# Kernel optimization log

Hardware: AMD Instinct MI355X
Metric: run time of the kernel (lower is better)

Reference implementation:

```python
import jax, jax.numpy as jnp
import numpy as np


def setup_inputs() -> dict:
    key = jax.random.key(0)
    ks = jax.random.split(key, 9)
    B, C, H, W = 16, 512, 64, 64
    C8 = C // 8
    s_in = 1.0 / np.sqrt(C)
    s_out = 1.0 / np.sqrt(C8)
    return {
        "x": jax.random.normal(ks[0], (B, C, H, W), dtype=jnp.float32),
        "Wq": jax.random.normal(ks[1], (C8, C), dtype=jnp.float32) * s_in,
        "bq": jax.random.normal(ks[2], (C8,), dtype=jnp.float32) * s_in,
        "Wk": jax.random.normal(ks[3], (C8, C), dtype=jnp.float32) * s_in,
        "bk": jax.random.normal(ks[4], (C8,), dtype=jnp.float32) * s_in,
        "Wv": jax.random.normal(ks[5], (C8, C), dtype=jnp.float32) * s_in,
        "bv": jax.random.normal(ks[6], (C8,), dtype=jnp.float32) * s_in,
        "Wo": jax.random.normal(ks[7], (C, C8), dtype=jnp.float32) * s_out,
        "bo": jax.random.normal(ks[8], (C,), dtype=jnp.float32) * s_out,
    }


def reference(x, Wq, bq, Wk, bk, Wv, bv, Wo, bo):
    B, C, H, W = x.shape
    N = H * W
    xf = x.reshape(B, C, N)  # 1x1 conv == channel matmul over flattened spatial
    q = jnp.einsum("oc,bcn->bon", Wq, xf) + bq[None, :, None]  # [B, C8, N]
    k = jnp.einsum("oc,bcn->bon", Wk, xf) + bk[None, :, None]
    v = jnp.einsum("oc,bcn->bon", Wv, xf) + bv[None, :, None]
    energy = jnp.einsum("bcn,bdn->bcd", q, k)  # [B, C8, C8] channel attention
    attn = jax.nn.softmax(energy, axis=-1)
    out = jnp.einsum("bcd,bdn->bcn", attn, v)  # [B, C8, N]
    out = jnp.einsum("oc,bcn->bon", Wo, out) + bo[None, :, None]  # [B, C, N]
    return out.reshape(B, C, H, W)
```

## Files before the change

kernel.cpp:

```cpp
#include <hip/hip_runtime.h>
#include <hip/hip_bf16.h>
#include <cstdint>

#define B_SZ 16
#define C_IN 512
#define C8   64
#define NSP  4096
#define QR   192

typedef __attribute__((ext_vector_type(8))) short s8v;
typedef __attribute__((ext_vector_type(4))) float f4v;

__device__ __forceinline__ void split_bf16(float x, unsigned short& h, unsigned short& l) {
    unsigned int u = __float_as_uint(x);
    h = (unsigned short)(u >> 16);
    float r = x - __uint_as_float(u & 0xffff0000u);
    l = (unsigned short)(__float_as_uint(r) >> 16);
}

__global__ __launch_bounds__(256) void k_convW(
    const float* __restrict__ Wq, const float* __restrict__ Wk,
    const float* __restrict__ Wv,
    unsigned short* __restrict__ whi, unsigned short* __restrict__ wlo)
{
    const int o = blockIdx.x;
    const float* src = (o < 64)  ? (Wq + (size_t)o * C_IN)
                     : (o < 128) ? (Wk + (size_t)(o - 64) * C_IN)
                                 : (Wv + (size_t)(o - 128) * C_IN);
    for (int c = threadIdx.x; c < C_IN; c += 256) {
        unsigned short h, l;
        split_bf16(src[c], h, l);
        whi[(size_t)o * C_IN + c] = h;
        wlo[(size_t)o * C_IN + c] = l;
    }
}

__global__ __launch_bounds__(512, 4) void k_qkv_mfma(
    const float* __restrict__ x,
    const unsigned short* __restrict__ whi, const unsigned short* __restrict__ wlo,
    const float* __restrict__ bq, const float* __restrict__ bk,
    const float* __restrict__ bv,
    float* __restrict__ qkv)
{
    __shared__ unsigned short as_h[QR * 32], as_l[QR * 32];
    __shared__ unsigned short xs_h[128 * 32], xs_l[128 * 32];

    const int b  = blockIdx.y;
    const int n0 = blockIdx.x * 128;
    const int t  = threadIdx.x;
    const int w  = t >> 6;
    const int l  = t & 63;
    const int wm = w >> 1;
    const int wn = w & 1;
    const int lm = l & 15;
    const int slot = (((l >> 4) ^ (l & 3)) << 3);

    const int nB    = t & 127;
    const int kgB   = t >> 7;
    const int slotB = ((kgB ^ (nB & 3)) << 3);

    f4v acc[3][4];
#pragma unroll
    for (int i = 0; i < 3; ++i)
#pragma unroll
        for (int j = 0; j < 4; ++j) acc[i][j] = (f4v)0.f;

    const float* xcol = x + ((size_t)b * C_IN) * NSP + n0 + nB;
    float xr[8];
    auto loadB = [&](int K0) {
        const float* s_ = xcol + (size_t)(K0 + kgB * 8) * NSP;
#pragma unroll
        for (int j = 0; j < 8; ++j) xr[j] = s_[(size_t)j * NSP];
    };
    loadB(0);

    for (int it = 0; it < 16; ++it) {
        const int k0 = it * 32;
        __syncthreads();
        {
            unsigned short h[8], lo[8];
#pragma unroll
            for (int j = 0; j < 8; ++j) split_bf16(xr[j], h[j], lo[j]);
            s8v hv, lv;
#pragma unroll
            for (int j = 0; j < 8; ++j) { hv[j] = (short)h[j]; lv[j] = (short)lo[j]; }
            *(s8v*)&xs_h[nB * 32 + slotB] = hv;
            *(s8v*)&xs_l[nB * 32 + slotB] = lv;
        }
        for (int c = t; c < 768; c += 512) {
            const int m = c >> 2, kga = c & 3;
            const int dst = m * 32 + ((kga ^ (m & 3)) << 3);
            const size_t srcoff = (size_t)m * C_IN + k0 + kga * 8;
            *(s8v*)&as_h[dst] = *(const s8v*)&whi[srcoff];
            *(s8v*)&as_l[dst] = *(const s8v*)&wlo[srcoff];
        }
        if (it < 15) loadB(k0 + 32);
        __syncthreads();
        s8v ah[3], al[3], bh[4], bl[4];
#pragma unroll
        for (int fm = 0; fm < 3; ++fm) {
            const int m = wm * 48 + fm * 16 + lm;
            ah[fm] = *(const s8v*)&as_h[m * 32 + slot];
            al[fm] = *(const s8v*)&as_l[m * 32 + slot];
        }
#pragma unroll
        for (int fn = 0; fn < 4; ++fn) {
            const int n = wn * 64 + fn * 16 + lm;
            bh[fn] = *(const s8v*)&xs_h[n * 32 + slot];
            bl[fn] = *(const s8v*)&xs_l[n * 32 + slot];
        }
#pragma unroll
        for (int fm = 0; fm < 3; ++fm)
#pragma unroll
            for (int fn = 0; fn < 4; ++fn) {
                acc[fm][fn] = __builtin_amdgcn_mfma_f32_16x16x32_bf16(
                    ah[fm], bh[fn], acc[fm][fn], 0, 0, 0);
                acc[fm][fn] = __builtin_amdgcn_mfma_f32_16x16x32_bf16(
                    ah[fm], bl[fn], acc[fm][fn], 0, 0, 0);
                acc[fm][fn] = __builtin_amdgcn_mfma_f32_16x16x32_bf16(
                    al[fm], bh[fn], acc[fm][fn], 0, 0, 0);
            }
    }

#pragma unroll
    for (int fm = 0; fm < 3; ++fm) {
        const int row0 = wm * 48 + fm * 16;
        const float* barr = (row0 < 64) ? bq : (row0 < 128) ? bk : bv;
        const int rbase = (row0 & 63) + (l >> 4) * 4;
        const int rowg  = row0 + (l >> 4) * 4;
#pragma unroll
        for (int fn = 0; fn < 4; ++fn) {
            const int col = n0 + wn * 64 + fn * 16 + lm;
            float* dst = qkv + ((size_t)b * QR + rowg) * NSP + col;
#pragma unroll
            for (int r = 0; r < 4; ++r)
                dst[(size_t)r * NSP] = acc[fm][fn][r] + barr[rbase + r];
        }
    }
}

__global__ __launch_bounds__(256) void k_energy(
    const float* __restrict__ qkv, float* __restrict__ part)
{
    __shared__ float qs[64][133];
    __shared__ float ks[64][133];
    const int b = blockIdx.y, s = blockIdx.x;
    const int n0 = s * 128;
    const int t = threadIdx.x;
    const int cg = t & 15, dg = t >> 4;
    const float* qb = qkv + (size_t)b * QR * NSP + n0;
    const float* kb = qb + (size_t)C8 * NSP;
#pragma unroll
    for (int i = 0; i < 8; ++i) {
        int idx = t + 256 * i;
        int c = idx >> 5, j4 = idx & 31;
        float4 qv = *reinterpret_cast<const float4*>(qb + (size_t)c * NSP + j4 * 4);
        float4 kv = *reinterpret_cast<const float4*>(kb + (size_t)c * NSP + j4 * 4);
        qs[c][j4 * 4 + 0] = qv.x; qs[c][j4 * 4 + 1] = qv.y;
        qs[c][j4 * 4 + 2] = qv.z; qs[c][j4 * 4 + 3] = qv.w;
        ks[c][j4 * 4 + 0] = kv.x; ks[c][j4 * 4 + 1] = kv.y;
        ks[c][j4 * 4 + 2] = kv.z; ks[c][j4 * 4 + 3] = kv.w;
    }
    __syncthreads();
    float acc[4][4];
#pragma unroll
    for (int i = 0; i < 4; ++i)
#pragma unroll
        for (int j = 0; j < 4; ++j) acc[i][j] = 0.f;
#pragma unroll 4
    for (int nn = 0; nn < 128; ++nn) {
        float qv[4], kv[4];
#pragma unroll
        for (int i = 0; i < 4; ++i) qv[i] = qs[cg * 4 + i][nn];
#pragma unroll
        for (int j = 0; j < 4; ++j) kv[j] = ks[dg * 4 + j][nn];
#pragma unroll
        for (int i = 0; i < 4; ++i)
#pragma unroll
            for (int j = 0; j < 4; ++j)
                acc[i][j] = fmaf(qv[i], kv[j], acc[i][j]);
    }
#pragma unroll
    for (int i = 0; i < 4; ++i) {
        float4 ov;
        ov.x = acc[i][0]; ov.y = acc[i][1]; ov.z = acc[i][2]; ov.w = acc[i][3];
        *reinterpret_cast<float4*>(
            part + (((size_t)b * 32 + s) * 64 + cg * 4 + i) * 64 + dg * 4) = ov;
    }
}

__global__ __launch_bounds__(256) void k_softmax(
    const float* __restrict__ part, float* __restrict__ attn)
{
    __shared__ float red[4][64];
    const int cRow = blockIdx.x, b = blockIdx.y;
    const int t = threadIdx.x, d = t & 63, sg = t >> 6;
    const float* p = part + (size_t)b * 32 * 4096 + cRow * 64 + d;
    float s = 0.f;
#pragma unroll
    for (int i = 0; i < 8; ++i) s += p[(size_t)(sg * 8 + i) * 4096];
    red[sg][d] = s;
    __syncthreads();
    if (t < 64) {
        float v = red[0][d] + red[1][d] + red[2][d] + red[3][d];
        float m = v;
#pragma unroll
        for (int off = 32; off; off >>= 1) m = fmaxf(m, __shfl_xor(m, off));
        float e = __expf(v - m);
        float sum = e;
#pragma unroll
        for (int off = 32; off; off >>= 1) sum += __shfl_xor(sum, off);
        attn[((size_t)b * 64 + cRow) * 64 + d] = e / sum;
    }
}

__global__ __launch_bounds__(256) void k_woattn(
    const float* __restrict__ Wo, const float* __restrict__ attn,
    float* __restrict__ Mmat)
{
    __shared__ float wosT[64][68];
    __shared__ float as[64][68];
    const int b  = blockIdx.y;
    const int o0 = blockIdx.x * 64;
    const int t  = threadIdx.x;
    const int td = t & 15, to = t >> 4;
#pragma unroll
    for (int i = 0; i < 4; ++i) {
        int idx = t + 256 * i;
        int r = idx >> 4, q4 = idx & 15;
        float4 w = *reinterpret_cast<const float4*>(
            Wo + (size_t)(o0 + r) * 64 + q4 * 4);
        wosT[q4 * 4 + 0][r] = w.x; wosT[q4 * 4 + 1][r] = w.y;
        wosT[q4 * 4 + 2][r] = w.z; wosT[q4 * 4 + 3][r] = w.w;
        float4 a = *reinterpret_cast<const float4*>(
            attn + ((size_t)b * 64 + r) * 64 + q4 * 4);
        *reinterpret_cast<float4*>(&as[r][q4 * 4]) = a;
    }
    __syncthreads();
    float acc[4][4];
#pragma unroll
    for (int i = 0; i < 4; ++i)
#pragma unroll
        for (int j = 0; j < 4; ++j) acc[i][j] = 0.f;
#pragma unroll 8
    for (int kk = 0; kk < 64; ++kk) {
        float4 wv = *reinterpret_cast<const float4*>(&wosT[kk][to * 4]);
        float4 av = *reinterpret_cast<const float4*>(&as[kk][td * 4]);
        const float wr[4] = {wv.x, wv.y, wv.z, wv.w};
        const float ar[4] = {av.x, av.y, av.z, av.w};
#pragma unroll
        for (int i = 0; i < 4; ++i)
#pragma unroll
            for (int j = 0; j < 4; ++j)
                acc[i][j] = fmaf(wr[i], ar[j], acc[i][j]);
    }
#pragma unroll
    for (int i = 0; i < 4; ++i) {
        float4 ov;
        ov.x = acc[i][0]; ov.y = acc[i][1]; ov.z = acc[i][2]; ov.w = acc[i][3];
        *reinterpret_cast<float4*>(
            Mmat + ((size_t)b * 512 + o0 + to * 4 + i) * 64 + td * 4) = ov;
    }
}

__global__ __launch_bounds__(256) void k_out(
    const float* __restrict__ qkv, const float* __restrict__ Mmat,
    const float* __restrict__ bo, float* __restrict__ out)
{
    __shared__ float vs[64][68];
    __shared__ float msT[64][68];
    const int b  = blockIdx.z;
    const int o0 = blockIdx.y * 64;
    const int n0 = blockIdx.x * 64;
    const int t  = threadIdx.x;
    const int tn = t & 15, to = t >> 4;
    const float* vb = qkv + ((size_t)b * QR + 128) * NSP + n0;
#pragma unroll
    for (int i = 0; i < 4; ++i) {
        int idx = t + 256 * i;
        int r = idx >> 4, q4 = idx & 15;
        float4 v = *reinterpret_cast<const float4*>(vb + (size_t)r * NSP + q4 * 4);
        *reinterpret_cast<float4*>(&vs[r][q4 * 4]) = v;
        float4 m = *reinterpret_cast<const float4*>(
            Mmat + ((size_t)b * 512 + o0 + r) * 64 + q4 * 4);
        msT[q4 * 4 + 0][r] = m.x; msT[q4 * 4 + 1][r] = m.y;
        msT[q4 * 4 + 2][r] = m.z; msT[q4 * 4 + 3][r] = m.w;
    }
    __syncthreads();
    float acc[4][4];
#pragma unroll
    for (int i = 0; i < 4; ++i)
#pragma unroll
        for (int j = 0; j < 4; ++j) acc[i][j] = 0.f;
#pragma unroll 8
    for (int kk = 0; kk < 64; ++kk) {
        float4 mv = *reinterpret_cast<const float4*>(&msT[kk][to * 4]);
        float4 vv = *reinterpret_cast<const float4*>(&vs[kk][tn * 4]);
        const float mr[4] = {mv.x, mv.y, mv.z, mv.w};
        const float vr[4] = {vv.x, vv.y, vv.z, vv.w};
#pragma unroll
        for (int i = 0; i < 4; ++i)
#pragma unroll
            for (int j = 0; j < 4; ++j)
                acc[i][j] = fmaf(mr[i], vr[j], acc[i][j]);
    }
#pragma unroll
    for (int i = 0; i < 4; ++i) {
        int o = o0 + to * 4 + i;
        float bias = bo[o];
        float4 ov;
        ov.x = acc[i][0] + bias; ov.y = acc[i][1] + bias;
        ov.z = acc[i][2] + bias; ov.w = acc[i][3] + bias;
        *reinterpret_cast<float4*>(
            out + ((size_t)b * 512 + o) * NSP + n0 + tn * 4) = ov;
    }
}

extern "C" void kernel_launch(void* const* d_in, const int* in_sizes, int n_in,
                              void* d_out, int out_size, void* d_ws, size_t ws_size,
                              hipStream_t stream)
{
    const float* x  = (const float*)d_in[0];
    const float* Wq = (const float*)d_in[1];
    const float* bq = (const float*)d_in[2];
    const float* Wk = (const float*)d_in[3];
    const float* bk = (const float*)d_in[4];
    const float* Wv = (const float*)d_in[5];
    const float* bv = (const float*)d_in[6];
    const float* Wo = (const float*)d_in[7];
    const float* bo = (const float*)d_in[8];
    float* out = (float*)d_out;

    float* ws   = (float*)d_ws;
    float* qkv  = ws;
    float* part = qkv  + (size_t)B_SZ * QR * NSP;
    float* attn = part + (size_t)B_SZ * 32 * 64 * 64;
    float* Mmat = attn + (size_t)B_SZ * 64 * 64;

    unsigned short* whi = (unsigned short*)part;
    unsigned short* wlo = whi + (size_t)QR * C_IN;

    k_convW   <<<dim3(QR),          256, 0, stream>>>(Wq, Wk, Wv, whi, wlo);
    k_qkv_mfma<<<dim3(32, B_SZ),    512, 0, stream>>>(x, whi, wlo, bq, bk, bv, qkv);
    k_energy  <<<dim3(32, B_SZ),    256, 0, stream>>>(qkv, part);
    k_softmax <<<dim3(64, B_SZ),    256, 0, stream>>>(part, attn);
    k_woattn  <<<dim3(8, B_SZ),     256, 0, stream>>>(Wo, attn, Mmat);
    k_out     <<<dim3(64, 8, B_SZ), 256, 0, stream>>>(qkv, Mmat, bo, out);
}
```

Before: 333.6 us.

## Port energy and output projection kernels to split-bf16 MFMA

Rewrites the energy (Q·K^T partials) and final output projection kernels to use bf16 MFMA instructions with a hi/lo split (three MFMAs per tile) in place of scalar FP32 FMAs. The output kernel now stages V transposed as bf16 hi/lo in an XOR-swizzled shared-memory layout and processes 128 spatial columns per block. The aim is to cut the FP32 ALU cost of these GEMMs while keeping near-FP32 accuracy. It adds split conversion overhead, and the output stores are now scalar strided writes instead of float4.

```diff
diff --git a/kernel.cpp b/kernel.cpp
--- a/kernel.cpp
+++ b/kernel.cpp
@@ -16,6 +16,15 @@
     h = (unsigned short)(u >> 16);
     float r = x - __uint_as_float(u & 0xffff0000u);
     l = (unsigned short)(__float_as_uint(r) >> 16);
+}
+
+__device__ __forceinline__ void split8(const float* v, s8v& h, s8v& l) {
+#pragma unroll
+    for (int j = 0; j < 8; ++j) {
+        unsigned short hh, ll;
+        split_bf16(v[j], hh, ll);
+        h[j] = (short)hh; l[j] = (short)ll;
+    }
 }
 
 __global__ __launch_bounds__(256) void k_convW(
@@ -139,54 +148,46 @@
     }
 }
 
-__global__ __launch_bounds__(256) void k_energy(
+__global__ __launch_bounds__(256) void k_energy_mfma(
     const float* __restrict__ qkv, float* __restrict__ part)
 {
-    __shared__ float qs[64][133];
-    __shared__ float ks[64][133];
     const int b = blockIdx.y, s = blockIdx.x;
-    const int n0 = s * 128;
-    const int t = threadIdx.x;
-    const int cg = t & 15, dg = t >> 4;
-    const float* qb = qkv + (size_t)b * QR * NSP + n0;
+    const int t = threadIdx.x, w = t >> 6, l = t & 63;
+    const int lm = l & 15, lq = l >> 4;
+    const float* qb = qkv + (size_t)b * QR * NSP + (size_t)s * 128;
     const float* kb = qb + (size_t)C8 * NSP;
-#pragma unroll
-    for (int i = 0; i < 8; ++i) {
-        int idx = t + 256 * i;
-        int c = idx >> 5, j4 = idx & 31;
-        float4 qv = *reinterpret_cast<const float4*>(qb + (size_t)c * NSP + j4 * 4);
-        float4 kv = *reinterpret_cast<const float4*>(kb + (size_t)c * NSP + j4 * 4);
-        qs[c][j4 * 4 + 0] = qv.x; qs[c][j4 * 4 + 1] = qv.y;
-        qs[c][j4 * 4 + 2] = qv.z; qs[c][j4 * 4 + 3] = qv.w;
-        ks[c][j4 * 4 + 0] = kv.x; ks[c][j4 * 4 + 1] = kv.y;
-        ks[c][j4 * 4 + 2] = kv.z; ks[c][j4 * 4 + 3] = kv.w;
-    }
-    __syncthreads();
-    float acc[4][4];
-#pragma unroll
-    for (int i = 0; i < 4; ++i)
-#pragma unroll
-        for (int j = 0; j < 4; ++j) acc[i][j] = 0.f;
-#pragma unroll 4
-    for (int nn = 0; nn < 128; ++nn) {
-        float qv[4], kv[4];
-#pragma unroll
-        for (int i = 0; i < 4; ++i) qv[i] = qs[cg * 4 + i][nn];
-#pragma unroll
-        for (int j = 0; j < 4; ++j) kv[j] = ks[dg * 4 + j][nn];
-#pragma unroll
-        for (int i = 0; i < 4; ++i)
-#pragma unroll
-            for (int j = 0; j < 4; ++j)
-                acc[i][j] = fmaf(qv[i], kv[j], acc[i][j]);
-    }
-#pragma unroll
-    for (int i = 0; i < 4; ++i) {
-        float4 ov;
-        ov.x = acc[i][0]; ov.y = acc[i][1]; ov.z = acc[i][2]; ov.w = acc[i][3];
-        *reinterpret_cast<float4*>(
-            part + (((size_t)b * 32 + s) * 64 + cg * 4 + i) * 64 + dg * 4) = ov;
-    }
+
+    f4v acc[4];
+#pragma unroll
+    for (int fd = 0; fd < 4; ++fd) acc[fd] = (f4v)0.f;
+
+#pragma unroll
+    for (int ks = 0; ks < 4; ++ks) {
+        const float* qrow = qb + (size_t)(w * 16 + lm) * NSP + ks * 32 + lq * 8;
+        float qv[8];
+        *(float4*)&qv[0] = *(const float4*)qrow;
+        *(float4*)&qv[4] = *(const float4*)(qrow + 4);
+        s8v qh, ql_;
+        split8(qv, qh, ql_);
+#pragma unroll
+        for (int fd = 0; fd < 4; ++fd) {
+            const float* krow = kb + (size_t)(fd * 16 + lm) * NSP + ks * 32 + lq * 8;
+            float kv[8];
+            *(float4*)&kv[0] = *(const float4*)krow;
+            *(float4*)&kv[4] = *(const float4*)(krow + 4);
+            s8v kh, kl_;
+            split8(kv, kh, kl_);
+            acc[fd] = __builtin_amdgcn_mfma_f32_16x16x32_bf16(qh, kh,  acc[fd], 0, 0, 0);
+            acc[fd] = __builtin_amdgcn_mfma_f32_16x16x32_bf16(qh, kl_, acc[fd], 0, 0, 0);
+            acc[fd] = __builtin_amdgcn_mfma_f32_16x16x32_bf16(ql_, kh, acc[fd], 0, 0, 0);
+        }
+    }
+    float* pb = part + ((size_t)b * 32 + s) * 4096;
+#pragma unroll
+    for (int fd = 0; fd < 4; ++fd)
+#pragma unroll
+        for (int r = 0; r < 4; ++r)
+            pb[(w * 16 + lq * 4 + r) * 64 + fd * 16 + lm] = acc[fd][r];
 }
 
 __global__ __launch_bounds__(256) void k_softmax(
@@ -263,56 +264,91 @@
     }
 }
 
-__global__ __launch_bounds__(256) void k_out(
+__global__ __launch_bounds__(256) void k_out_mfma(
     const float* __restrict__ qkv, const float* __restrict__ Mmat,
     const float* __restrict__ bo, float* __restrict__ out)
 {
-    __shared__ float vs[64][68];
-    __shared__ float msT[64][68];
+    __shared__ unsigned short vsT_h[128 * 64];
+    __shared__ unsigned short vsT_l[128 * 64];
     const int b  = blockIdx.z;
     const int o0 = blockIdx.y * 64;
-    const int n0 = blockIdx.x * 64;
+    const int n0 = blockIdx.x * 128;
     const int t  = threadIdx.x;
-    const int tn = t & 15, to = t >> 4;
-    const float* vb = qkv + ((size_t)b * QR + 128) * NSP + n0;
-#pragma unroll
-    for (int i = 0; i < 4; ++i) {
-        int idx = t + 256 * i;
-        int r = idx >> 4, q4 = idx & 15;
-        float4 v = *reinterpret_cast<const float4*>(vb + (size_t)r * NSP + q4 * 4);
-        *reinterpret_cast<float4*>(&vs[r][q4 * 4]) = v;
-        float4 m = *reinterpret_cast<const float4*>(
-            Mmat + ((size_t)b * 512 + o0 + r) * 64 + q4 * 4);
-        msT[q4 * 4 + 0][r] = m.x; msT[q4 * 4 + 1][r] = m.y;
-        msT[q4 * 4 + 2][r] = m.z; msT[q4 * 4 + 3][r] = m.w;
-    }
+    const int w  = t >> 6, l = t & 63;
+    const int lm = l & 15, lq = l >> 4;
+
+    const float* vb = qkv + ((size_t)b * QR + 128) * NSP;
+
+#pragma unroll
+    for (int s = 0; s < 2; ++s)
+#pragma unroll
+        for (int dd = 0; dd < 16; ++dd) {
+            const int d = w + 4 * dd;
+            const int n = 64 * s + l;
+            float xv = vb[(size_t)d * NSP + n0 + n];
+            unsigned short h, lo_;
+            split_bf16(xv, h, lo_);
+            const int addr = n * 64 + ((((d >> 3) ^ (n & 7))) << 3) + (d & 7);
+            vsT_h[addr] = h;
+            vsT_l[addr] = lo_;
+        }
+
+    s8v ah[4][2], al[4][2];
+#pragma unroll
+    for (int fo = 0; fo < 4; ++fo)
+#pragma unroll
+        for (int ks = 0; ks < 2; ++ks) {
+            const float* mrow = Mmat + ((size_t)b * 512 + o0 + fo * 16 + lm) * 64
+                                + ks * 32 + lq * 8;
+            float mv[8];
+            *(float4*)&mv[0] = *(const float4*)mrow;
+            *(float4*)&mv[4] = *(const float4*)(mrow + 4);
+            split8(mv, ah[fo][ks], al[fo][ks]);
+        }
     __syncthreads();
-    float acc[4][4];
-#pragma unroll
-    for (int i = 0; i < 4; ++i)
-#pragma unroll
-        for (int j = 0; j < 4; ++j) acc[i][j] = 0.f;
-#pragma unroll 8
-    for (int kk = 0; kk < 64; ++kk) {
-        float4 mv = *reinterpret_cast<const float4*>(&msT[kk][to * 4]);
-        float4 vv = *reinterpret_cast<const float4*>(&vs[kk][tn * 4]);
-        const float mr[4] = {mv.x, mv.y, mv.z, mv.w};
-        const float vr[4] = {vv.x, vv.y, vv.z, vv.w};
-#pragma unroll
-        for (int i = 0; i < 4; ++i)
-#pragma unroll
-            for (int j = 0; j < 4; ++j)
-                acc[i][j] = fmaf(mr[i], vr[j], acc[i][j]);
-    }
-#pragma unroll
-    for (int i = 0; i < 4; ++i) {
-        int o = o0 + to * 4 + i;
-        float bias = bo[o];
-        float4 ov;
-        ov.x = acc[i][0] + bias; ov.y = acc[i][1] + bias;
-        ov.z = acc[i][2] + bias; ov.w = acc[i][3] + bias;
-        *reinterpret_cast<float4*>(
-            out + ((size_t)b * 512 + o) * NSP + n0 + tn * 4) = ov;
+
+    f4v acc[4][2];
+#pragma unroll
+    for (int fo = 0; fo < 4; ++fo)
+#pragma unroll
+        for (int fn = 0; fn < 2; ++fn) acc[fo][fn] = (f4v)0.f;
+
+    const int nwbase = w * 32;
+#pragma unroll
+    for (int ks = 0; ks < 2; ++ks) {
+        s8v bh[2], bl[2];
+#pragma unroll
+        for (int fn = 0; fn < 2; ++fn) {
+            const int n = nwbase + fn * 16 + lm;
+            const int slot = (ks * 4 + lq) ^ (n & 7);
+            const int addr = n * 64 + (slot << 3);
+            bh[fn] = *(const s8v*)&vsT_h[addr];
+            bl[fn] = *(const s8v*)&vsT_l[addr];
+        }
+#pragma unroll
+        for (int fo = 0; fo < 4; ++fo)
+#pragma unroll
+            for (int fn = 0; fn < 2; ++fn) {
+                acc[fo][fn] = __builtin_amdgcn_mfma_f32_16x16x32_bf16(
+                    ah[fo][ks], bh[fn], acc[fo][fn], 0, 0, 0);
+                acc[fo][fn] = __builtin_amdgcn_mfma_f32_16x16x32_bf16(
+                    ah[fo][ks], bl[fn], acc[fo][fn], 0, 0, 0);
+                acc[fo][fn] = __builtin_amdgcn_mfma_f32_16x16x32_bf16(
+                    al[fo][ks], bh[fn], acc[fo][fn], 0, 0, 0);
+            }
+    }
+
+#pragma unroll
+    for (int fo = 0; fo < 4; ++fo) {
+        const int orow0 = o0 + fo * 16 + lq * 4;
+#pragma unroll
+        for (int fn = 0; fn < 2; ++fn) {
+            const int col = n0 + nwbase + fn * 16 + lm;
+            float* dst = out + ((size_t)b * 512 + orow0) * NSP + col;
+#pragma unroll
+            for (int r = 0; r < 4; ++r)
+                dst[(size_t)r * NSP] = acc[fo][fn][r] + bo[orow0 + r];
+        }
     }
 }
 
@@ -340,10 +376,10 @@
     unsigned short* whi = (unsigned short*)part;
     unsigned short* wlo = whi + (size_t)QR * C_IN;
 
-    k_convW   <<<dim3(QR),          256, 0, stream>>>(Wq, Wk, Wv, whi, wlo);
-    k_qkv_mfma<<<dim3(32, B_SZ),    512, 0, stream>>>(x, whi, wlo, bq, bk, bv, qkv);
-    k_energy  <<<dim3(32, B_SZ),    256, 0, stream>>>(qkv, part);
-    k_softmax <<<dim3(64, B_SZ),    256, 0, stream>>>(part, attn);
-    k_woattn  <<<dim3(8, B_SZ),     256, 0, stream>>>(Wo, attn, Mmat);
-    k_out     <<<dim3(64, 8, B_SZ), 256, 0, stream>>>(qkv, Mmat, bo, out);
-}
+    k_convW      <<<dim3(QR),          256, 0, stream>>>(Wq, Wk, Wv, whi, wlo);
+    k_qkv_mfma   <<<dim3(32, B_SZ),    512, 0, stream>>>(x, whi, wlo, bq, bk, bv, qkv);
+    k_energy_mfma<<<dim3(32, B_SZ),    256, 0, stream>>>(qkv, part);
+    k_softmax    <<<dim3(64, B_SZ),    256, 0, stream>>>(part, attn);
+    k_woattn     <<<dim3(8, B_SZ),     256, 0, stream>>>(Wo, attn, Mmat);
+    k_out_mfma   <<<dim3(32, 8, B_SZ), 256, 0, stream>>>(qkv, Mmat, bo, out);
+}
```

Result: faster. 308.6 us (-7.5%).
